# Kernel optimization log

Hardware: AMD Instinct MI355X
Metric: run time of the kernel (lower is better)

## Reference

```python
import jax, jax.numpy as jnp
import numpy as np

B, C, H, W = 4, 96, 256, 256
WS = 8          # window size
NH = 4          # num heads
SHIFT = 4       # shift size (block_idx=1 -> WS//2)
HD = C // NH    # head dim = 24
N = WS * WS     # tokens per window = 64
MLP_H = 4 * C   # 384
EPS = 1e-6


def _rel_pos_index():
    coords = np.stack(np.meshgrid(np.arange(WS), np.arange(WS), indexing='ij'))  # [2,WS,WS]
    cf = coords.reshape(2, -1)                                                   # [2,N]
    rel = cf[:, :, None] - cf[:, None, :]                                        # [2,N,N]
    rel = rel.transpose(1, 2, 0) + (WS - 1)
    rel[:, :, 0] *= 2 * WS - 1
    return rel.sum(-1)  # [N,N] int


def _attn_mask():
    # standard Swin shifted-window mask, static (numpy)
    img = np.zeros((H, W), dtype=np.float32)
    cnt = 0
    for hs in (slice(0, -WS), slice(-WS, -SHIFT), slice(-SHIFT, None)):
        for ws_ in (slice(0, -WS), slice(-WS, -SHIFT), slice(-SHIFT, None)):
            img[hs, ws_] = cnt
            cnt += 1
    m = img.reshape(H // WS, WS, W // WS, WS).transpose(0, 2, 1, 3).reshape(-1, N)  # [nW,N]
    am = m[:, None, :] - m[:, :, None]
    return np.where(am != 0, -100.0, 0.0).astype(np.float32)  # [nW,N,N]


REL_IDX = _rel_pos_index()
ATTN_MASK = _attn_mask()


def _ln(x, w, b):
    mu = x.mean(-1, keepdims=True)
    var = ((x - mu) ** 2).mean(-1, keepdims=True)
    return (x - mu) * jax.lax.rsqrt(var + EPS) * w + b


def setup_inputs() -> dict:
    key = jax.random.key(0)
    ks = jax.random.split(key, 8)
    s = 0.02
    return {
        'x': jax.random.normal(ks[0], (B, C, H, W), jnp.float32),
        'norm_w': jnp.ones((C,), jnp.float32),
        'norm_b': jnp.zeros((C,), jnp.float32),
        'qkv_w': jax.random.normal(ks[1], (3 * C, C), jnp.float32) * s,
        'qkv_b': jnp.zeros((3 * C,), jnp.float32),
        'proj_w': jax.random.normal(ks[2], (C, C), jnp.float32) * s,
        'proj_b': jnp.zeros((C,), jnp.float32),
        'rpb_table': jax.random.normal(ks[3], ((2 * WS - 1) ** 2, NH), jnp.float32) * s,
        'norm2_w': jnp.ones((C,), jnp.float32),
        'norm2_b': jnp.zeros((C,), jnp.float32),
        'fc1_w': jax.random.normal(ks[4], (MLP_H, C), jnp.float32) * s,
        'fc1_b': jnp.zeros((MLP_H,), jnp.float32),
        'fc2_w': jax.random.normal(ks[5], (C, MLP_H), jnp.float32) * s,
        'fc2_b': jnp.zeros((C,), jnp.float32),
    }


def _swin_msa(y, qkv_w, qkv_b, proj_w, proj_b, rpb_table):
    # y: [B,H,W,C] (already layer-normed)
    ys = jnp.roll(y, shift=(-SHIFT, -SHIFT), axis=(1, 2))
    nWh, nWw = H // WS, W // WS
    # window partition -> [B*nW, N, C]
    xw = ys.reshape(B, nWh, WS, nWw, WS, C).transpose(0, 1, 3, 2, 4, 5).reshape(-1, N, C)
    qkv = xw @ qkv_w.T + qkv_b                       # [Bn,N,3C]
    qkv = qkv.reshape(-1, N, 3, NH, HD).transpose(2, 0, 3, 1, 4)  # [3,Bn,NH,N,HD]
    q, k, v = qkv[0], qkv[1], qkv[2]
    scale = HD ** -0.5
    attn = jnp.einsum('bhnd,bhmd->bhnm', q * scale, k)           # [Bn,NH,N,N]
    bias = rpb_table[jnp.asarray(REL_IDX)].transpose(2, 0, 1)    # [NH,N,N]
    attn = attn + bias[None]
    nW = nWh * nWw
    mask = jnp.asarray(ATTN_MASK)                                # [nW,N,N]
    attn = attn.reshape(B, nW, NH, N, N) + mask[None, :, None]
    attn = jax.nn.softmax(attn.reshape(-1, NH, N, N), axis=-1)
    out = jnp.einsum('bhnm,bhmd->bhnd', attn, v)                 # [Bn,NH,N,HD]
    out = out.transpose(0, 2, 1, 3).reshape(-1, N, C)
    out = out @ proj_w.T + proj_b
    # window reverse
    out = out.reshape(B, nWh, nWw, WS, WS, C).transpose(0, 1, 3, 2, 4, 5).reshape(B, H, W, C)
    return jnp.roll(out, shift=(SHIFT, SHIFT), axis=(1, 2))


def reference(x, norm_w, norm_b, qkv_w, qkv_b, proj_w, proj_b, rpb_table,
              norm2_w, norm2_b, fc1_w, fc1_b, fc2_w, fc2_b):
    xp = x.transpose(0, 2, 3, 1)                                  # [B,H,W,C]
    h = xp + _swin_msa(_ln(xp, norm_w, norm_b), qkv_w, qkv_b, proj_w, proj_b, rpb_table)
    y2 = _ln(h, norm2_w, norm2_b)
    mlp = jax.nn.gelu(y2 @ fc1_w.T + fc1_b, approximate=False) @ fc2_w.T + fc2_b
    h = h + mlp                                                   # proj is Identity (in==out)
    return h.transpose(0, 3, 1, 2)
```

## Files before the change

### kernel.cpp

```cpp
#include <hip/hip_runtime.h>
#include <hip/hip_bf16.h>
#include <math.h>

constexpr int B_    = 4;
constexpr int C_    = 96;
constexpr int H_    = 256;
constexpr int W_    = 256;
constexpr int WS_   = 8;
constexpr int NH_   = 4;
constexpr int SHIFT_= 4;
constexpr int HD_   = 24;
constexpr int HW_   = H_*W_;
constexpr float EPS_   = 1e-6f;
constexpr float SCALE_ = 0.20412414523193150f;

using bf16   = __bf16;
using bf16x8 = __attribute__((ext_vector_type(8))) __bf16;
using bf16x4 = __attribute__((ext_vector_type(4))) __bf16;
using f32x4  = __attribute__((ext_vector_type(4))) float;

__device__ __forceinline__ f32x4 mfma16(bf16x8 a, bf16x8 b, f32x4 c) {
    return __builtin_amdgcn_mfma_f32_16x16x32_bf16(a, b, c, 0, 0, 0);
}

constexpr int    WQ2_E   = 320*96;
constexpr int    WPR_E   = 96*96;
constexpr int    WF1_E   = 384*96;
constexpr int    WF2_E   = 96*384;
constexpr int    WSUM_E  = WQ2_E + WPR_E + WF1_E + WF2_E;
constexpr int    NBQ     = 320;
constexpr int    WBLKS   = (WSUM_E + NBQ + 255)/256;

__global__ __launch_bounds__(256) void prepw_kernel(
    const float* __restrict__ qkv_w, const float* __restrict__ qkv_b,
    const float* __restrict__ proj_w, const float* __restrict__ fc1w,
    const float* __restrict__ fc2w,
    bf16* __restrict__ warena, float* __restrict__ bq2)
{
    int i = blockIdx.x*256 + threadIdx.x;
    if (i < WQ2_E) {
        int R = i/96, c = i%96;
        int h = R/80, s = R%80;
        float v;
        if      (s < 24) v = qkv_w[(h*24+s)*96 + c] * SCALE_;
        else if (s < 48) v = qkv_w[(96 + h*24 + s-24)*96 + c];
        else if (s < 72) v = qkv_w[(192 + h*24 + s-48)*96 + c];
        else             v = 0.f;
        warena[i] = (bf16)v;
    } else if (i < WQ2_E + WPR_E) {
        warena[i] = (bf16)proj_w[i - WQ2_E];
    } else if (i < WQ2_E + WPR_E + WF1_E) {
        warena[i] = (bf16)fc1w[i - WQ2_E - WPR_E];
    } else if (i < WSUM_E) {
        warena[i] = (bf16)fc2w[i - WQ2_E - WPR_E - WF1_E];
    } else if (i < WSUM_E + NBQ) {
        int j = i - WSUM_E;
        int h = j/80, s = j%80;
        float v;
        if      (s < 24) v = qkv_b[h*24+s] * SCALE_;
        else if (s < 48) v = qkv_b[96 + h*24 + s-24];
        else if (s < 72) v = qkv_b[192 + h*24 + s-48];
        else             v = 0.f;
        bq2[j] = v;
    }
}

constexpr int AXO_E = 0;
constexpr int SCR_E = 6656;
constexpr int ASQ_E = SCR_E;
constexpr int ASK_E = SCR_E + 2560;
constexpr int ASV_E = SCR_E + 4096;
constexpr int ASP_E = SCR_E + 5824;
constexpr int MYG_E = SCR_E;
constexpr int SM_E  = SCR_E + 10432;

__global__ __launch_bounds__(256, 2) void fused_kernel(
    const float* __restrict__ x,
    const float* __restrict__ norm_w, const float* __restrict__ norm_b,
    const bf16*  __restrict__ wq2,
    const float* __restrict__ bq2,
    const bf16*  __restrict__ wproj,
    const float* __restrict__ proj_b,
    const float* __restrict__ rpb,
    const float* __restrict__ n2w, const float* __restrict__ n2b,
    const bf16*  __restrict__ wfc1, const float* __restrict__ fc1b,
    const bf16*  __restrict__ wfc2, const float* __restrict__ fc2b,
    float* __restrict__ out)
{
    __shared__ __align__(16) bf16 sm[SM_E];

    const int tid  = threadIdx.x;
    const int wave = tid >> 6, lane = tid & 63;
    const int l16  = lane & 15, quad = lane >> 4;
    const int t  = tid >> 2, qa = tid & 3;
    const int qrow0 = wave*16;

    const int blk = blockIdx.x;
    const int b   = blk >> 10;
    const int wid = blk & 1023;
    const int wh  = wid >> 5, ww = wid & 31;

    #pragma unroll
    for (int it = 0; it < 6; ++it) {
        const int i2  = it*256 + tid;
        const int c   = i2 >> 4;
        const int rem = i2 & 15;
        const int wi  = rem >> 1;
        const int wj4 = (rem & 1)*4;
        const int gh  = (wh*WS_ + wi + SHIFT_) & (H_-1);
        const int gw0 = (ww*WS_ + wj4 + SHIFT_) & (W_-1);
        f32x4 v4 = *(const f32x4*)(x + (size_t)(b*96 + c)*HW_ + gh*W_ + gw0);
        #pragma unroll
        for (int j = 0; j < 4; ++j)
            sm[AXO_E + (wi*8 + wj4 + j)*104 + c] = (bf16)v4[j];
    }
    __syncthreads();

    bf16x8 xreg[3];
    {
        float v[24]; float mu = 0.f, ss = 0.f;
        #pragma unroll
        for (int k = 0; k < 3; ++k) {
            xreg[k] = *(const bf16x8*)&sm[AXO_E + t*104 + qa*24 + k*8];
            #pragma unroll
            for (int j = 0; j < 8; ++j) {
                v[k*8+j] = (float)xreg[k][j];
                mu += v[k*8+j]; ss += v[k*8+j]*v[k*8+j];
            }
        }
        mu += __shfl_xor(mu,1); mu += __shfl_xor(mu,2);
        ss += __shfl_xor(ss,1); ss += __shfl_xor(ss,2);
        mu *= (1.f/C_);
        float rstd = rsqrtf(ss*(1.f/C_) - mu*mu + EPS_);
        #pragma unroll
        for (int k = 0; k < 3; ++k) {
            bf16x8 ln8;
            #pragma unroll
            for (int j = 0; j < 8; ++j) {
                const int c = qa*24 + k*8 + j;
                ln8[j] = (bf16)((v[k*8+j]-mu)*rstd*norm_w[c] + norm_b[c]);
            }
            *(bf16x8*)&sm[AXO_E + t*104 + qa*24 + k*8] = ln8;
        }
    }
    __syncthreads();

    if (tid < 64) { bf16x8 z = {}; *(bf16x8*)&sm[ASQ_E + tid*40 + 24] = z; }

    bf16x8 af[4][3];
    #pragma unroll
    for (int mt = 0; mt < 4; ++mt)
        #pragma unroll
        for (int kk = 0; kk < 3; ++kk)
            af[mt][kk] = *(const bf16x8*)&sm[AXO_E + (mt*16+l16)*104 + kk*32 + quad*8];

    for (int h = 0; h < NH_; ++h) {
        for (int jt = 0; jt < 5; ++jt) {
            if (((h*5 + jt) & 3) != wave) continue;
            const int s   = jt*16 + l16;
            const int row = h*80 + s;
            bf16x8 bw[3];
            #pragma unroll
            for (int kk = 0; kk < 3; ++kk)
                bw[kk] = *(const bf16x8*)(wq2 + (size_t)row*96 + kk*32 + quad*8);
            const float bias = bq2[row];
            #pragma unroll
            for (int mt = 0; mt < 4; ++mt) {
                f32x4 acc = {};
                #pragma unroll
                for (int kk = 0; kk < 3; ++kk) acc = mfma16(af[mt][kk], bw[kk], acc);
                const int tb = mt*16 + quad*4;
                if (s < 24) {
                    #pragma unroll
                    for (int r = 0; r < 4; ++r)
                        sm[ASQ_E + (tb+r)*40 + s] = (bf16)(acc[r] + bias);
                } else if (s < 48) {
                    #pragma unroll
                    for (int r = 0; r < 4; ++r)
                        sm[ASK_E + (tb+r)*24 + (s-24)] = (bf16)(acc[r] + bias);
                } else if (s < 72) {
                    bf16x4 pv;
                    #pragma unroll
                    for (int r = 0; r < 4; ++r) pv[r] = (bf16)(acc[r] + bias);
                    *(bf16x4*)&sm[ASV_E + (s-48)*72 + tb] = pv;
                }
            }
        }
        __syncthreads();

        bf16x8 aq = *(const bf16x8*)&sm[ASQ_E + (qrow0 + l16)*40 + quad*8];
        f32x4 accS[4];
        #pragma unroll
        for (int kt = 0; kt < 4; ++kt) {
            bf16x8 bk = *(const bf16x8*)&sm[ASK_E + (kt*16+l16)*24 + quad*8];
            f32x4 z = {};
            accS[kt] = mfma16(aq, bk, z);
        }
        float s_[4][4];
        #pragma unroll
        for (int kt = 0; kt < 4; ++kt) {
            const int key = kt*16 + l16;
            const int ki = key >> 3, kj = key & 7;
            const int labk = (((wh*8+ki) >= H_-WS_) + ((wh*8+ki) >= H_-SHIFT_))*3
                           +  ((ww*8+kj) >= W_-WS_) + ((ww*8+kj) >= W_-SHIFT_);
            #pragma unroll
            for (int r = 0; r < 4; ++r) {
                const int q = qrow0 + quad*4 + r;
                const int ti = q >> 3, tj = q & 7;
                const int labq = (((wh*8+ti) >= H_-WS_) + ((wh*8+ti) >= H_-SHIFT_))*3
                               +  ((ww*8+tj) >= W_-WS_) + ((ww*8+tj) >= W_-SHIFT_);
                const int ridx = (ti - ki + 7)*15 + (tj - kj + 7);
                float val = accS[kt][r] + rpb[ridx*NH_ + h];
                if (labk != labq) val -= 100.f;
                s_[kt][r] = val;
            }
        }
        #pragma unroll
        for (int r = 0; r < 4; ++r) {
            float m = fmaxf(fmaxf(s_[0][r], s_[1][r]), fmaxf(s_[2][r], s_[3][r]));
            m = fmaxf(m, __shfl_xor(m,1)); m = fmaxf(m, __shfl_xor(m,2));
            m = fmaxf(m, __shfl_xor(m,4)); m = fmaxf(m, __shfl_xor(m,8));
            float su = 0.f;
            #pragma unroll
            for (int kt = 0; kt < 4; ++kt) { s_[kt][r] = __expf(s_[kt][r]-m); su += s_[kt][r]; }
            su += __shfl_xor(su,1); su += __shfl_xor(su,2);
            su += __shfl_xor(su,4); su += __shfl_xor(su,8);
            const float inv = 1.f/su;
            #pragma unroll
            for (int kt = 0; kt < 4; ++kt)
                sm[ASP_E + (qrow0 + quad*4 + r)*72 + kt*16 + l16] = (bf16)(s_[kt][r]*inv);
        }
        __syncthreads();

        bf16x8 ap0 = *(const bf16x8*)&sm[ASP_E + (qrow0+l16)*72 + quad*8];
        bf16x8 ap1 = *(const bf16x8*)&sm[ASP_E + (qrow0+l16)*72 + 32 + quad*8];
        #pragma unroll
        for (int nt2 = 0; nt2 < 2; ++nt2) {
            const int d = nt2*16 + l16;
            bf16x8 bv0 = *(const bf16x8*)&sm[ASV_E + d*72 + quad*8];
            bf16x8 bv1 = *(const bf16x8*)&sm[ASV_E + d*72 + 32 + quad*8];
            f32x4 acc = {};
            acc = mfma16(ap0, bv0, acc);
            acc = mfma16(ap1, bv1, acc);
            if (d < HD_) {
                #pragma unroll
                for (int r = 0; r < 4; ++r)
                    sm[AXO_E + (qrow0 + quad*4 + r)*104 + h*24 + d] = (bf16)acc[r];
            }
        }
        __syncthreads();
    }

    {
        bf16x8 ao[3];
        #pragma unroll
        for (int kk = 0; kk < 3; ++kk)
            ao[kk] = *(const bf16x8*)&sm[AXO_E + (qrow0 + l16)*104 + kk*32 + quad*8];
        for (int nt = 0; nt < 6; ++nt) {
            const int oc = nt*16 + l16;
            bf16x8 bw[3];
            #pragma unroll
            for (int kk = 0; kk < 3; ++kk)
                bw[kk] = *(const bf16x8*)(wproj + (size_t)oc*96 + kk*32 + quad*8);
            f32x4 acc = {};
            #pragma unroll
            for (int kk = 0; kk < 3; ++kk) acc = mfma16(ao[kk], bw[kk], acc);
            #pragma unroll
            for (int r = 0; r < 4; ++r)
                sm[AXO_E + (qrow0 + quad*4 + r)*104 + oc] = (bf16)acc[r];
        }
    }
    __syncthreads();

    {
        float hv[24]; float mu = 0.f, ss = 0.f;
        #pragma unroll
        for (int k = 0; k < 3; ++k) {
            bf16x8 po = *(const bf16x8*)&sm[AXO_E + t*104 + qa*24 + k*8];
            bf16x8 h8;
            #pragma unroll
            for (int j = 0; j < 8; ++j) {
                float hf = (float)xreg[k][j] + (float)po[j] + proj_b[qa*24 + k*8 + j];
                h8[j] = (bf16)hf;
                float hb = (float)h8[j];
                hv[k*8+j] = hb;
                mu += hb; ss += hb*hb;
            }
            *(bf16x8*)&sm[AXO_E + t*104 + qa*24 + k*8] = h8;
        }
        mu += __shfl_xor(mu,1); mu += __shfl_xor(mu,2);
        ss += __shfl_xor(ss,1); ss += __shfl_xor(ss,2);
        mu *= (1.f/C_);
        float rstd = rsqrtf(ss*(1.f/C_) - mu*mu + EPS_);
        #pragma unroll
        for (int k = 0; k < 3; ++k) {
            bf16x8 o;
            #pragma unroll
            for (int j = 0; j < 8; ++j) {
                const int c = qa*24 + k*8 + j;
                o[j] = (bf16)((hv[k*8+j]-mu)*rstd*n2w[c] + n2b[c]);
            }
            *(bf16x8*)&sm[MYG_E + t*104 + qa*24 + k*8] = o;
        }
    }
    __syncthreads();

    bf16x8 af2[4][3];
    #pragma unroll
    for (int mt = 0; mt < 4; ++mt)
        #pragma unroll
        for (int kk = 0; kk < 3; ++kk)
            af2[mt][kk] = *(const bf16x8*)&sm[MYG_E + (mt*16+l16)*104 + kk*32 + quad*8];
    __syncthreads();

    f32x4 acc2[6];
    #pragma unroll
    for (int n = 0; n < 6; ++n) acc2[n] = (f32x4){};

    for (int ci = 0; ci < 3; ++ci) {
        #pragma unroll
        for (int rep = 0; rep < 2; ++rep) {
            const int ntl = wave + rep*4;
            const int ub  = ci*128 + ntl*16;
            bf16x8 bw[3];
            #pragma unroll
            for (int kk = 0; kk < 3; ++kk)
                bw[kk] = *(const bf16x8*)(wfc1 + (size_t)(ub + l16)*96 + kk*32 + quad*8);
            const f32x4 b4 = *(const f32x4*)&fc1b[ub + quad*4];
            #pragma unroll
            for (int mt = 0; mt < 4; ++mt) {
                f32x4 acc = {};
                #pragma unroll
                for (int kk = 0; kk < 3; ++kk) acc = mfma16(bw[kk], af2[mt][kk], acc);
                bf16x4 g4;
                #pragma unroll
                for (int r = 0; r < 4; ++r) {
                    float tv = acc[r] + b4[r];
                    float uu = tv*tv;
                    float w  = tv*fmaf(-0.0713548165f, uu, -1.5957691216f);
                    float e  = __expf(w);
                    g4[r] = (bf16)(tv*__builtin_amdgcn_rcpf(1.f + e));
                }
                *(bf16x4*)&sm[MYG_E + (mt*16 + l16)*136 + ntl*16 + quad*4] = g4;
            }
        }
        __syncthreads();
        bf16x8 ag[4];
        #pragma unroll
        for (int kq = 0; kq < 4; ++kq)
            ag[kq] = *(const bf16x8*)&sm[MYG_E + (wave*16+l16)*136 + kq*32 + quad*8];
        #pragma unroll
        for (int nt2 = 0; nt2 < 6; ++nt2) {
            const int c = nt2*16 + l16;
            #pragma unroll
            for (int kq = 0; kq < 4; ++kq) {
                bf16x8 bw = *(const bf16x8*)(wfc2 + (size_t)c*384 + ci*128 + kq*32 + quad*8);
                acc2[nt2] = mfma16(ag[kq], bw, acc2[nt2]);
            }
        }
        if (ci < 2) __syncthreads();
    }

    {
        const int row = wave*16 + quad*4;
        const int gh  = (wh*WS_ + (row>>3) + SHIFT_) & (H_-1);
        const int gw0 = (ww*WS_ + (row&7)  + SHIFT_) & (W_-1);
        #pragma unroll
        for (int nt2 = 0; nt2 < 6; ++nt2) {
            const int c = nt2*16 + l16;
            const float bias = fc2b[c];
            f32x4 o;
            #pragma unroll
            for (int r = 0; r < 4; ++r)
                o[r] = acc2[nt2][r] + bias + (float)sm[AXO_E + (row+r)*104 + c];
            *(f32x4*)(out + (size_t)(b*96 + c)*HW_ + gh*W_ + gw0) = o;
        }
    }
}

extern "C" void kernel_launch(void* const* d_in, const int* in_sizes, int n_in,
                              void* d_out, int out_size, void* d_ws, size_t ws_size,
                              hipStream_t stream) {
    const float* x      = (const float*)d_in[0];
    const float* norm_w = (const float*)d_in[1];
    const float* norm_b = (const float*)d_in[2];
    const float* qkv_w  = (const float*)d_in[3];
    const float* qkv_b  = (const float*)d_in[4];
    const float* proj_w = (const float*)d_in[5];
    const float* proj_b = (const float*)d_in[6];
    const float* rpb    = (const float*)d_in[7];
    const float* n2w    = (const float*)d_in[8];
    const float* n2b    = (const float*)d_in[9];
    const float* fc1w   = (const float*)d_in[10];
    const float* fc1b   = (const float*)d_in[11];
    const float* fc2w   = (const float*)d_in[12];
    const float* fc2b   = (const float*)d_in[13];

    float* outp = (float*)d_out;
    char*  ws   = (char*)d_ws;
    bf16*  wa   = (bf16*)ws;
    float* bq2  = (float*)(ws + (size_t)WSUM_E*2);

    prepw_kernel<<<WBLKS, 256, 0, stream>>>(qkv_w, qkv_b, proj_w, fc1w, fc2w, wa, bq2);
    fused_kernel<<<B_*1024, 256, 0, stream>>>(x, norm_w, norm_b,
                                              wa, bq2,
                                              wa + WQ2_E, proj_b, rpb,
                                              n2w, n2b,
                                              wa + WQ2_E + WPR_E, fc1b,
                                              wa + WQ2_E + WPR_E + WF1_E, fc2b,
                                              outp);
}
```

Measured before the change: 529.6 us.

## Double-buffer per-head QKV in LDS and hoist mask/bias index computation

Per-head Q/K/V buffers in shared memory are now double-buffered, so the QKV projection for the next head runs while the current head's attention is computed. This removes one block-wide barrier per head. The relative-position index and shift-mask terms are computed once before the head loop instead of once per head. Launch bounds are raised to 3 blocks per CU, but shared memory grows from about 34 KB to about 46 KB per block, and the hoisted index and mask arrays add register pressure, so occupancy may fall short of that target.

```diff
diff --git a/kernel.cpp b/kernel.cpp
--- a/kernel.cpp
+++ b/kernel.cpp
@@ -66,15 +66,13 @@
 }
 
 constexpr int AXO_E = 0;
-constexpr int SCR_E = 6656;
-constexpr int ASQ_E = SCR_E;
-constexpr int ASK_E = SCR_E + 2560;
-constexpr int ASV_E = SCR_E + 4096;
-constexpr int ASP_E = SCR_E + 5824;
-constexpr int MYG_E = SCR_E;
-constexpr int SM_E  = SCR_E + 10432;
-
-__global__ __launch_bounds__(256, 2) void fused_kernel(
+constexpr int B0_E  = 6656;
+constexpr int B1_E  = 12480;
+constexpr int P_E   = 18304;
+constexpr int MYG_E = 6656;
+constexpr int SM_E  = 22912;
+
+__global__ __launch_bounds__(256, 3) void fused_kernel(
     const float* __restrict__ x,
     const float* __restrict__ norm_w, const float* __restrict__ norm_b,
     const bf16*  __restrict__ wq2,
@@ -145,7 +143,11 @@
     }
     __syncthreads();
 
-    if (tid < 64) { bf16x8 z = {}; *(bf16x8*)&sm[ASQ_E + tid*40 + 24] = z; }
+    if (tid < 128) {
+        bf16x8 z = {};
+        const int bb = (tid >> 6) ? B1_E : B0_E;
+        *(bf16x8*)&sm[bb + (tid & 63)*40 + 24] = z;
+    }
 
     bf16x8 af[4][3];
     #pragma unroll
@@ -154,11 +156,31 @@
         for (int kk = 0; kk < 3; ++kk)
             af[mt][kk] = *(const bf16x8*)&sm[AXO_E + (mt*16+l16)*104 + kk*32 + quad*8];
 
-    for (int h = 0; h < NH_; ++h) {
+    int   rix[4][4];
+    float mb [4][4];
+    #pragma unroll
+    for (int kt = 0; kt < 4; ++kt) {
+        const int key = kt*16 + l16;
+        const int ki = key >> 3, kj = key & 7;
+        const int labk = (((wh*8+ki) >= H_-WS_) + ((wh*8+ki) >= H_-SHIFT_))*3
+                       +  ((ww*8+kj) >= W_-WS_) + ((ww*8+kj) >= W_-SHIFT_);
+        #pragma unroll
+        for (int r = 0; r < 4; ++r) {
+            const int q = qrow0 + quad*4 + r;
+            const int ti = q >> 3, tj = q & 7;
+            const int labq = (((wh*8+ti) >= H_-WS_) + ((wh*8+ti) >= H_-SHIFT_))*3
+                           +  ((ww*8+tj) >= W_-WS_) + ((ww*8+tj) >= W_-SHIFT_);
+            rix[kt][r] = ((ti - ki + 7)*15 + (tj - kj + 7))*NH_;
+            mb [kt][r] = (labk != labq) ? -100.f : 0.f;
+        }
+    }
+
+    auto qkv_head = [&](int hh, int qb) {
+        #pragma unroll
         for (int jt = 0; jt < 5; ++jt) {
-            if (((h*5 + jt) & 3) != wave) continue;
+            if (((hh*5 + jt) & 3) != wave) continue;
             const int s   = jt*16 + l16;
-            const int row = h*80 + s;
+            const int row = hh*80 + s;
             bf16x8 bw[3];
             #pragma unroll
             for (int kk = 0; kk < 3; ++kk)
@@ -173,48 +195,44 @@
                 if (s < 24) {
                     #pragma unroll
                     for (int r = 0; r < 4; ++r)
-                        sm[ASQ_E + (tb+r)*40 + s] = (bf16)(acc[r] + bias);
+                        sm[qb + (tb+r)*40 + s] = (bf16)(acc[r] + bias);
                 } else if (s < 48) {
                     #pragma unroll
                     for (int r = 0; r < 4; ++r)
-                        sm[ASK_E + (tb+r)*24 + (s-24)] = (bf16)(acc[r] + bias);
+                        sm[qb + 2560 + (tb+r)*24 + (s-24)] = (bf16)(acc[r] + bias);
                 } else if (s < 72) {
                     bf16x4 pv;
                     #pragma unroll
                     for (int r = 0; r < 4; ++r) pv[r] = (bf16)(acc[r] + bias);
-                    *(bf16x4*)&sm[ASV_E + (s-48)*72 + tb] = pv;
+                    *(bf16x4*)&sm[qb + 4096 + (s-48)*72 + tb] = pv;
                 }
             }
         }
-        __syncthreads();
-
-        bf16x8 aq = *(const bf16x8*)&sm[ASQ_E + (qrow0 + l16)*40 + quad*8];
+    };
+
+    qkv_head(0, B0_E);
+    __syncthreads();
+
+    for (int h = 0; h < NH_; ++h) {
+        const int cb = (h & 1) ? B1_E : B0_E;
+        const int nb = (h & 1) ? B0_E : B1_E;
+
+        if (h < NH_-1) qkv_head(h+1, nb);
+
+        bf16x8 aq = *(const bf16x8*)&sm[cb + (qrow0 + l16)*40 + quad*8];
         f32x4 accS[4];
         #pragma unroll
         for (int kt = 0; kt < 4; ++kt) {
-            bf16x8 bk = *(const bf16x8*)&sm[ASK_E + (kt*16+l16)*24 + quad*8];
+            bf16x8 bk = *(const bf16x8*)&sm[cb + 2560 + (kt*16+l16)*24 + quad*8];
             f32x4 z = {};
             accS[kt] = mfma16(aq, bk, z);
         }
         float s_[4][4];
         #pragma unroll
-        for (int kt = 0; kt < 4; ++kt) {
-            const int key = kt*16 + l16;
-            const int ki = key >> 3, kj = key & 7;
-            const int labk = (((wh*8+ki) >= H_-WS_) + ((wh*8+ki) >= H_-SHIFT_))*3
-                           +  ((ww*8+kj) >= W_-WS_) + ((ww*8+kj) >= W_-SHIFT_);
-            #pragma unroll
-            for (int r = 0; r < 4; ++r) {
-                const int q = qrow0 + quad*4 + r;
-                const int ti = q >> 3, tj = q & 7;
-                const int labq = (((wh*8+ti) >= H_-WS_) + ((wh*8+ti) >= H_-SHIFT_))*3
-                               +  ((ww*8+tj) >= W_-WS_) + ((ww*8+tj) >= W_-SHIFT_);
-                const int ridx = (ti - ki + 7)*15 + (tj - kj + 7);
-                float val = accS[kt][r] + rpb[ridx*NH_ + h];
-                if (labk != labq) val -= 100.f;
-                s_[kt][r] = val;
-            }
-        }
+        for (int kt = 0; kt < 4; ++kt)
+            #pragma unroll
+            for (int r = 0; r < 4; ++r)
+                s_[kt][r] = accS[kt][r] + rpb[rix[kt][r] + h] + mb[kt][r];
         #pragma unroll
         for (int r = 0; r < 4; ++r) {
             float m = fmaxf(fmaxf(s_[0][r], s_[1][r]), fmaxf(s_[2][r], s_[3][r]));
@@ -228,17 +246,17 @@
             const float inv = 1.f/su;
             #pragma unroll
             for (int kt = 0; kt < 4; ++kt)
-                sm[ASP_E + (qrow0 + quad*4 + r)*72 + kt*16 + l16] = (bf16)(s_[kt][r]*inv);
+                sm[P_E + (qrow0 + quad*4 + r)*72 + kt*16 + l16] = (bf16)(s_[kt][r]*inv);
         }
         __syncthreads();
 
-        bf16x8 ap0 = *(const bf16x8*)&sm[ASP_E + (qrow0+l16)*72 + quad*8];
-        bf16x8 ap1 = *(const bf16x8*)&sm[ASP_E + (qrow0+l16)*72 + 32 + quad*8];
+        bf16x8 ap0 = *(const bf16x8*)&sm[P_E + (qrow0+l16)*72 + quad*8];
+        bf16x8 ap1 = *(const bf16x8*)&sm[P_E + (qrow0+l16)*72 + 32 + quad*8];
         #pragma unroll
         for (int nt2 = 0; nt2 < 2; ++nt2) {
             const int d = nt2*16 + l16;
-            bf16x8 bv0 = *(const bf16x8*)&sm[ASV_E + d*72 + quad*8];
-            bf16x8 bv1 = *(const bf16x8*)&sm[ASV_E + d*72 + 32 + quad*8];
+            bf16x8 bv0 = *(const bf16x8*)&sm[cb + 4096 + d*72 + quad*8];
+            bf16x8 bv1 = *(const bf16x8*)&sm[cb + 4096 + d*72 + 32 + quad*8];
             f32x4 acc = {};
             acc = mfma16(ap0, bv0, acc);
             acc = mfma16(ap1, bv1, acc);
```

Result: slower. 561.6 us (+6.0%).
